# Kernel optimization log

Hardware: AMD Instinct MI355X
Metric: run time of the kernel (lower is better)

The kernel has to match this reference:

```python
import jax, jax.numpy as jnp
import numpy as np

B, N, C_IN, C_OUT, K = 8, 1024, 64, 64, 4


def setup_inputs() -> dict:
    key = jax.random.key(0)
    k1, k2, k3 = jax.random.split(key, 3)
    x = jax.random.normal(k1, (B, N, C_IN), dtype=jnp.float32)
    # scaled-Laplacian-like matrix; 1/sqrt(N) scaling keeps Chebyshev recurrence stable
    L = jax.random.normal(k2, (B, N, N), dtype=jnp.float32) * (1.0 / np.sqrt(N))
    theta = jax.random.normal(k3, (K, C_IN, C_OUT), dtype=jnp.float32) * np.sqrt(2.0 / C_IN)
    return {"x": x, "L": L, "theta": theta}


def reference(x, L, theta):
    # Chebyshev recurrence applied directly to feature vectors:
    #   z0 = x, z1 = L x, z_k = 2 L z_{k-1} - z_{k-2}
    # out = sum_k z_k @ theta[k]  -- same math as materializing T_k(L),
    # since T_k(L) @ x obeys the same 3-term recurrence.
    k_orders = theta.shape[0]
    z_prev = x                      # [B,N,C]
    out = jnp.matmul(z_prev, theta[0])
    if k_orders > 1:
        z_curr = jnp.matmul(L, x)   # [B,N,C]
        out = out + jnp.matmul(z_curr, theta[1])
        for k in range(2, k_orders):
            z_next = 2.0 * jnp.matmul(L, z_curr) - z_prev
            out = out + jnp.matmul(z_next, theta[k])
            z_prev, z_curr = z_curr, z_next
    return out
```

## Files before the change

kernel.cpp:

```cpp
#include <hip/hip_runtime.h>
#include <cstdint>
#include <cstddef>


typedef __bf16 bf16;
typedef bf16 bf16x4 __attribute__((ext_vector_type(4)));
typedef bf16 bf16x8 __attribute__((ext_vector_type(8)));
typedef float f32x4 __attribute__((ext_vector_type(4)));

#define MFMA_BF16(a, b, c) __builtin_amdgcn_mfma_f32_16x16x32_bf16((a), (b), (c), 0, 0, 0)
#define WAITV(n) asm volatile("s_waitcnt vmcnt(" #n ")" ::: "memory")

__device__ __forceinline__ void dma16(const void* g, void* l) {
    __builtin_amdgcn_global_load_lds(
        (const __attribute__((address_space(1))) unsigned int*)g,
        (__attribute__((address_space(3))) unsigned int*)l, 16, 0, 0);
}

__global__ __launch_bounds__(256) void prep_kernel(const float* __restrict__ x,
                                                   const float* __restrict__ theta,
                                                   const float* __restrict__ Lmat,
                                                   bf16* __restrict__ xT,
                                                   bf16* __restrict__ xb,
                                                   bf16* __restrict__ thT,
                                                   bf16* __restrict__ Lb)
{
    const int bid = blockIdx.x;
    const int t = threadIdx.x;

    if (bid >= 132) {
        constexpr int CHUNKS = (8 * 1024 * 1024) / 4;
        const int stride = (1156 - 132) * 256;
        for (int idx = (bid - 132) * 256 + t; idx < CHUNKS; idx += stride) {
            f32x4 v = ((const f32x4*)Lmat)[idx];
            bf16x4 q;
#pragma unroll
            for (int i = 0; i < 4; ++i) q[i] = (bf16)v[i];
            ((bf16x4*)Lb)[idx] = q;
        }
        return;
    }

    __shared__ bf16 tile[64][72];
    const int r = t >> 2;
    const int c0 = (t & 3) << 4;
    const float* src;
    bf16* dstT;
    int dst_ld;
    const bool isx = bid < 128;
    int b = 0, n0 = 0;
    if (isx) {
        b = bid >> 4; n0 = (bid & 15) << 6;
        src = x + (size_t)(b * 1024 + n0) * 64;
        dstT = xT + (size_t)b * 64 * 1024 + n0;
        dst_ld = 1024;
    } else {
        const int k = bid - 128;
        src = theta + (size_t)k * 4096;
        dstT = thT + (size_t)k * 4096;
        dst_ld = 64;
    }

    bf16x8 row0, row1;
#pragma unroll
    for (int j = 0; j < 16; j += 4) {
        f32x4 v = *reinterpret_cast<const f32x4*>(src + r * 64 + c0 + j);
#pragma unroll
        for (int i = 0; i < 4; ++i) {
            bf16 q = (bf16)v[i];
            tile[r][c0 + j + i] = q;
            if (j + i < 8) row0[j + i] = q; else row1[j + i - 8] = q;
        }
    }
    if (isx) {
        bf16* xr = xb + (size_t)(b * 1024 + n0 + r) * 64 + c0;
        *reinterpret_cast<bf16x8*>(xr) = row0;
        *reinterpret_cast<bf16x8*>(xr + 8) = row1;
    }
    __syncthreads();
    bf16x8 o0, o1;
#pragma unroll
    for (int j = 0; j < 8; ++j) { o0[j] = tile[c0 + j][r]; o1[j] = tile[c0 + 8 + j][r]; }
    *reinterpret_cast<bf16x8*>(dstT + (size_t)r * dst_ld + c0) = o0;
    *reinterpret_cast<bf16x8*>(dstT + (size_t)r * dst_ld + c0 + 8) = o1;
}

template <int STAGE>
__global__ __launch_bounds__(256) void stage_kernel(
    const bf16* __restrict__ Lb,
    const bf16* __restrict__ xb,
    const bf16* __restrict__ zinT,
    const bf16* __restrict__ zprevT,
    const bf16* __restrict__ thT,
    bf16* __restrict__ zoutT,
    float* __restrict__ out)
{
    constexpr int D = 5, T = 16, KS = 64, LSTG = 10240;
    __shared__ __align__(16) unsigned char smem[D * LSTG + 16 * 72 * 2];

    const int bid = blockIdx.x;
    const int b  = bid >> 6;
    const int m0 = (bid & 63) << 4;
    const int t  = threadIdx.x;
    const int w  = t >> 6;
    const int l  = t & 63;
    const int l15 = l & 15;
    const int lg  = l >> 4;
    const int c0  = w << 4;

    const bf16* Lrb = Lb + ((size_t)(b * 1024 + m0)) * 1024;
    const bf16* zb  = zinT + (size_t)b * 64 * 1024;

    const int Lg = (w << 5) + (l & 31);
    const int Lrow = Lg >> 3, Lslot = Lg & 7;
    const bf16* Lsrc = Lrb + (size_t)Lrow * 1024 + (Lslot ^ (Lrow & 7)) * 8;
    const int Zg0 = (w << 7) + l, Zg1 = Zg0 + 64;
    const int Zch0 = Zg0 >> 3, Zch1 = Zg1 >> 3;
    const bf16* Zsrc0 = zb + (size_t)Zch0 * 1024 + ((Zg0 & 7) ^ (Zch0 & 7)) * 8;
    const bf16* Zsrc1 = zb + (size_t)Zch1 * 1024 + ((Zg1 & 7) ^ (Zch1 & 7)) * 8;

    auto issue = [&](int k0, unsigned char* bufb) {
        dma16(Zsrc0 + k0, bufb + 2048 + (w << 11));
        dma16(Zsrc1 + k0, bufb + 2048 + (w << 11) + 1024);
        if (l < 32)
            dma16(Lsrc + k0, bufb + (w << 9));
    };

    f32x4 acc = {0.f, 0.f, 0.f, 0.f};

    auto computeStep = [&](const unsigned char* bufb) {
        const bf16* Ll = (const bf16*)bufb;
        const bf16* Zl = (const bf16*)(bufb + 2048);
        const int chan = c0 + l15;
        const int sA = chan & 7;
        bf16x8 a0 = *(const bf16x8*)(Zl + (((chan << 3) + (lg ^ sA)) << 3));
        bf16x8 a1 = *(const bf16x8*)(Zl + (((chan << 3) + ((4 + lg) ^ sA)) << 3));
        const int sB = l15 & 7;
        bf16x8 b0 = *(const bf16x8*)(Ll + (((l15 << 3) + (lg ^ sB)) << 3));
        bf16x8 b1 = *(const bf16x8*)(Ll + (((l15 << 3) + ((4 + lg) ^ sB)) << 3));
        acc = MFMA_BF16(a0, b0, acc);
        acc = MFMA_BF16(a1, b1, acc);
    };

#pragma unroll
    for (int s = 0; s < D - 1; ++s)
        issue(s * KS, smem + s * LSTG);

#pragma unroll
    for (int tt = 0; tt < T; ++tt) {
        const int rem = (T - 1 - tt) < (D - 2) ? (T - 1 - tt) : (D - 2);
        if (rem >= 3)      WAITV(9);
        else if (rem == 2) WAITV(6);
        else if (rem == 1) WAITV(3);
        else               WAITV(0);
        __builtin_amdgcn_sched_barrier(0);
        __builtin_amdgcn_s_barrier();
        __builtin_amdgcn_sched_barrier(0);
        computeStep(smem + (tt % D) * LSTG);
        if (tt + D - 1 < T)
            issue((tt + D - 1) * KS, smem + ((tt + D - 1) % D) * LSTG);
    }

    bf16 (*zbuf)[72] = (bf16(*)[72])(smem + D * LSTG);
    const int cr = c0 + (lg << 2);
    const float alpha = (STAGE == 1) ? 1.0f : 2.0f;
    float zv[4];
#pragma unroll
    for (int r = 0; r < 4; ++r) {
        float zp = 0.f;
        if constexpr (STAGE >= 2)
            zp = (float)zprevT[(size_t)(b * 64 + cr + r) * 1024 + m0 + l15];
        zv[r] = alpha * acc[r] - zp;
    }
    if constexpr (STAGE <= 2) {
#pragma unroll
        for (int r = 0; r < 4; ++r)
            zoutT[(size_t)(b * 64 + cr + r) * 1024 + m0 + l15] = (bf16)zv[r];
    }
#pragma unroll
    for (int r = 0; r < 4; ++r)
        zbuf[l15][cr + r] = (bf16)zv[r];
    __syncthreads();

    const int o = (w << 4) + l15;
    f32x4 oacc;
    if constexpr (STAGE == 1) {
        oacc = (f32x4){0.f, 0.f, 0.f, 0.f};
#pragma unroll
        for (int ck = 0; ck < 2; ++ck) {
            bf16x8 ax = *reinterpret_cast<const bf16x8*>(
                xb + (size_t)(b * 1024 + m0 + l15) * 64 + ck * 32 + lg * 8);
            bf16x8 bt = *reinterpret_cast<const bf16x8*>(
                thT + (size_t)o * 64 + ck * 32 + lg * 8);
            oacc = MFMA_BF16(ax, bt, oacc);
        }
    } else {
#pragma unroll
        for (int r = 0; r < 4; ++r)
            oacc[r] = out[(size_t)(b * 1024 + m0 + lg * 4 + r) * 64 + o];
    }
    constexpr int KTH = (STAGE == 1) ? 1 : STAGE;
#pragma unroll
    for (int ck = 0; ck < 2; ++ck) {
        bf16x8 az = *reinterpret_cast<const bf16x8*>(&zbuf[l15][ck * 32 + lg * 8]);
        bf16x8 bt = *reinterpret_cast<const bf16x8*>(
            thT + (size_t)(KTH * 64 + o) * 64 + ck * 32 + lg * 8);
        oacc = MFMA_BF16(az, bt, oacc);
    }
#pragma unroll
    for (int r = 0; r < 4; ++r)
        out[(size_t)(b * 1024 + m0 + lg * 4 + r) * 64 + o] = oacc[r];
}

extern "C" void kernel_launch(void* const* d_in, const int* in_sizes, int n_in,
                              void* d_out, int out_size, void* d_ws, size_t ws_size,
                              hipStream_t stream)
{
    const float* x  = (const float*)d_in[0];
    const float* L  = (const float*)d_in[1];
    const float* th = (const float*)d_in[2];
    float* out = (float*)d_out;

    bf16* xT  = (bf16*)d_ws;
    bf16* xb  = xT  + (size_t)8 * 64 * 1024;
    bf16* z1T = xb  + (size_t)8 * 64 * 1024;
    bf16* z2T = z1T + (size_t)8 * 64 * 1024;
    bf16* thT = z2T + (size_t)8 * 64 * 1024;
    bf16* Lb  = thT + (size_t)4 * 64 * 64;

    prep_kernel<<<dim3(1156), dim3(256), 0, stream>>>(x, th, L, xT, xb, thT, Lb);
    stage_kernel<1><<<dim3(512), dim3(256), 0, stream>>>(Lb, xb, xT, nullptr, thT, z1T, out);
    stage_kernel<2><<<dim3(512), dim3(256), 0, stream>>>(Lb, xb, z1T, xT, thT, z2T, out);
    stage_kernel<3><<<dim3(512), dim3(256), 0, stream>>>(Lb, xb, z2T, z1T, thT, nullptr, out);
}
```

Baseline: 101.7 us.

## Double row tile per block to reuse Z loads, widen L conversion vectors

Result: no change. 99.73 us (-1.9%).

```diff
diff --git a/kernel.cpp b/kernel.cpp
--- a/kernel.cpp
+++ b/kernel.cpp
@@ -4,7 +4,6 @@
 
 
 typedef __bf16 bf16;
-typedef bf16 bf16x4 __attribute__((ext_vector_type(4)));
 typedef bf16 bf16x8 __attribute__((ext_vector_type(8)));
 typedef float f32x4 __attribute__((ext_vector_type(4)));
 
@@ -29,14 +28,15 @@
     const int t = threadIdx.x;
 
     if (bid >= 132) {
-        constexpr int CHUNKS = (8 * 1024 * 1024) / 4;
+        constexpr int CHUNKS = (8 * 1024 * 1024) / 8;
         const int stride = (1156 - 132) * 256;
         for (int idx = (bid - 132) * 256 + t; idx < CHUNKS; idx += stride) {
-            f32x4 v = ((const f32x4*)Lmat)[idx];
-            bf16x4 q;
-#pragma unroll
-            for (int i = 0; i < 4; ++i) q[i] = (bf16)v[i];
-            ((bf16x4*)Lb)[idx] = q;
+            f32x4 v0 = ((const f32x4*)Lmat)[2 * idx];
+            f32x4 v1 = ((const f32x4*)Lmat)[2 * idx + 1];
+            bf16x8 q;
+#pragma unroll
+            for (int i = 0; i < 4; ++i) { q[i] = (bf16)v0[i]; q[4 + i] = (bf16)v1[i]; }
+            ((bf16x8*)Lb)[idx] = q;
         }
         return;
     }
@@ -86,7 +86,7 @@
 }
 
 template <int STAGE>
-__global__ __launch_bounds__(256) void stage_kernel(
+__global__ __launch_bounds__(512) void stage_kernel(
     const bf16* __restrict__ Lb,
     const bf16* __restrict__ xb,
     const bf16* __restrict__ zinT,
@@ -95,18 +95,19 @@
     bf16* __restrict__ zoutT,
     float* __restrict__ out)
 {
-    constexpr int D = 5, T = 16, KS = 64, LSTG = 10240;
-    __shared__ __align__(16) unsigned char smem[D * LSTG + 16 * 72 * 2];
+    constexpr int D = 5, T = 16, KS = 64, LSTG = 12288;
+    __shared__ __align__(16) unsigned char smem[D * LSTG];
 
     const int bid = blockIdx.x;
-    const int b  = bid >> 6;
-    const int m0 = (bid & 63) << 4;
+    const int b  = bid >> 5;
+    const int m0 = (bid & 31) << 5;
     const int t  = threadIdx.x;
     const int w  = t >> 6;
     const int l  = t & 63;
     const int l15 = l & 15;
     const int lg  = l >> 4;
-    const int c0  = w << 4;
+    const int wq  = w & 3;
+    const int h   = w >> 2;
 
     const bf16* Lrb = Lb + ((size_t)(b * 1024 + m0)) * 1024;
     const bf16* zb  = zinT + (size_t)b * 64 * 1024;
@@ -114,14 +115,12 @@
     const int Lg = (w << 5) + (l & 31);
     const int Lrow = Lg >> 3, Lslot = Lg & 7;
     const bf16* Lsrc = Lrb + (size_t)Lrow * 1024 + (Lslot ^ (Lrow & 7)) * 8;
-    const int Zg0 = (w << 7) + l, Zg1 = Zg0 + 64;
-    const int Zch0 = Zg0 >> 3, Zch1 = Zg1 >> 3;
-    const bf16* Zsrc0 = zb + (size_t)Zch0 * 1024 + ((Zg0 & 7) ^ (Zch0 & 7)) * 8;
-    const bf16* Zsrc1 = zb + (size_t)Zch1 * 1024 + ((Zg1 & 7) ^ (Zch1 & 7)) * 8;
+    const int Zg = (w << 6) + l;
+    const int Zch = Zg >> 3;
+    const bf16* Zsrc = zb + (size_t)Zch * 1024 + ((Zg & 7) ^ (Zch & 7)) * 8;
 
     auto issue = [&](int k0, unsigned char* bufb) {
-        dma16(Zsrc0 + k0, bufb + 2048 + (w << 11));
-        dma16(Zsrc1 + k0, bufb + 2048 + (w << 11) + 1024);
+        dma16(Zsrc + k0, bufb + 4096 + (w << 10));
         if (l < 32)
             dma16(Lsrc + k0, bufb + (w << 9));
     };
@@ -130,14 +129,15 @@
 
     auto computeStep = [&](const unsigned char* bufb) {
         const bf16* Ll = (const bf16*)bufb;
-        const bf16* Zl = (const bf16*)(bufb + 2048);
-        const int chan = c0 + l15;
+        const bf16* Zl = (const bf16*)(bufb + 4096);
+        const int chan = (wq << 4) + l15;
         const int sA = chan & 7;
         bf16x8 a0 = *(const bf16x8*)(Zl + (((chan << 3) + (lg ^ sA)) << 3));
         bf16x8 a1 = *(const bf16x8*)(Zl + (((chan << 3) + ((4 + lg) ^ sA)) << 3));
-        const int sB = l15 & 7;
-        bf16x8 b0 = *(const bf16x8*)(Ll + (((l15 << 3) + (lg ^ sB)) << 3));
-        bf16x8 b1 = *(const bf16x8*)(Ll + (((l15 << 3) + ((4 + lg) ^ sB)) << 3));
+        const int mrow = (h << 4) + l15;
+        const int sB = mrow & 7;
+        bf16x8 b0 = *(const bf16x8*)(Ll + (((mrow << 3) + (lg ^ sB)) << 3));
+        bf16x8 b1 = *(const bf16x8*)(Ll + (((mrow << 3) + ((4 + lg) ^ sB)) << 3));
         acc = MFMA_BF16(a0, b0, acc);
         acc = MFMA_BF16(a1, b1, acc);
     };
@@ -148,10 +148,10 @@
 
 #pragma unroll
     for (int tt = 0; tt < T; ++tt) {
-        const int rem = (T - 1 - tt) < (D - 2) ? (T - 1 - tt) : (D - 2);
-        if (rem >= 3)      WAITV(9);
-        else if (rem == 2) WAITV(6);
-        else if (rem == 1) WAITV(3);
+        const int rem = ((T - tt) < (D - 1) ? (T - tt) : (D - 1)) - 1;
+        if (rem >= 3)      WAITV(6);
+        else if (rem == 2) WAITV(4);
+        else if (rem == 1) WAITV(2);
         else               WAITV(0);
         __builtin_amdgcn_sched_barrier(0);
         __builtin_amdgcn_s_barrier();
@@ -161,35 +161,37 @@
             issue((tt + D - 1) * KS, smem + ((tt + D - 1) % D) * LSTG);
     }
 
-    bf16 (*zbuf)[72] = (bf16(*)[72])(smem + D * LSTG);
-    const int cr = c0 + (lg << 2);
+    bf16 (*zbuf)[72] = (bf16(*)[72])(smem + LSTG);
+    const int cr   = (wq << 4) + (lg << 2);
+    const int mcol = m0 + (h << 4) + l15;
     const float alpha = (STAGE == 1) ? 1.0f : 2.0f;
     float zv[4];
 #pragma unroll
     for (int r = 0; r < 4; ++r) {
         float zp = 0.f;
         if constexpr (STAGE >= 2)
-            zp = (float)zprevT[(size_t)(b * 64 + cr + r) * 1024 + m0 + l15];
+            zp = (float)zprevT[(size_t)(b * 64 + cr + r) * 1024 + mcol];
         zv[r] = alpha * acc[r] - zp;
     }
     if constexpr (STAGE <= 2) {
 #pragma unroll
         for (int r = 0; r < 4; ++r)
-            zoutT[(size_t)(b * 64 + cr + r) * 1024 + m0 + l15] = (bf16)zv[r];
+            zoutT[(size_t)(b * 64 + cr + r) * 1024 + mcol] = (bf16)zv[r];
     }
 #pragma unroll
     for (int r = 0; r < 4; ++r)
-        zbuf[l15][cr + r] = (bf16)zv[r];
+        zbuf[(h << 4) + l15][cr + r] = (bf16)zv[r];
     __syncthreads();
 
-    const int o = (w << 4) + l15;
+    const int o = (wq << 4) + l15;
+    const int mrowA = m0 + (h << 4) + l15;
     f32x4 oacc;
     if constexpr (STAGE == 1) {
         oacc = (f32x4){0.f, 0.f, 0.f, 0.f};
 #pragma unroll
         for (int ck = 0; ck < 2; ++ck) {
             bf16x8 ax = *reinterpret_cast<const bf16x8*>(
-                xb + (size_t)(b * 1024 + m0 + l15) * 64 + ck * 32 + lg * 8);
+                xb + (size_t)(b * 1024 + mrowA) * 64 + ck * 32 + lg * 8);
             bf16x8 bt = *reinterpret_cast<const bf16x8*>(
                 thT + (size_t)o * 64 + ck * 32 + lg * 8);
             oacc = MFMA_BF16(ax, bt, oacc);
@@ -197,19 +199,20 @@
     } else {
 #pragma unroll
         for (int r = 0; r < 4; ++r)
-            oacc[r] = out[(size_t)(b * 1024 + m0 + lg * 4 + r) * 64 + o];
+            oacc[r] = out[(size_t)(b * 1024 + m0 + (h << 4) + lg * 4 + r) * 64 + o];
     }
     constexpr int KTH = (STAGE == 1) ? 1 : STAGE;
 #pragma unroll
     for (int ck = 0; ck < 2; ++ck) {
-        bf16x8 az = *reinterpret_cast<const bf16x8*>(&zbuf[l15][ck * 32 + lg * 8]);
+        bf16x8 az = *reinterpret_cast<const bf16x8*>(
+            &zbuf[(h << 4) + l15][ck * 32 + lg * 8]);
         bf16x8 bt = *reinterpret_cast<const bf16x8*>(
             thT + (size_t)(KTH * 64 + o) * 64 + ck * 32 + lg * 8);
         oacc = MFMA_BF16(az, bt, oacc);
     }
 #pragma unroll
     for (int r = 0; r < 4; ++r)
-        out[(size_t)(b * 1024 + m0 + lg * 4 + r) * 64 + o] = oacc[r];
+        out[(size_t)(b * 1024 + m0 + (h << 4) + lg * 4 + r) * 64 + o] = oacc[r];
 }
 
 extern "C" void kernel_launch(void* const* d_in, const int* in_sizes, int n_in,
@@ -229,7 +232,7 @@
     bf16* Lb  = thT + (size_t)4 * 64 * 64;
 
     prep_kernel<<<dim3(1156), dim3(256), 0, stream>>>(x, th, L, xT, xb, thT, Lb);
-    stage_kernel<1><<<dim3(512), dim3(256), 0, stream>>>(Lb, xb, xT, nullptr, thT, z1T, out);
-    stage_kernel<2><<<dim3(512), dim3(256), 0, stream>>>(Lb, xb, z1T, xT, thT, z2T, out);
-    stage_kernel<3><<<dim3(512), dim3(256), 0, stream>>>(Lb, xb, z2T, z1T, thT, nullptr, out);
-}
+    stage_kernel<1><<<dim3(256), dim3(512), 0, stream>>>(Lb, xb, xT, nullptr, thT, z1T, out);
+    stage_kernel<2><<<dim3(256), dim3(512), 0, stream>>>(Lb, xb, z1T, xT, thT, z2T, out);
+    stage_kernel<3><<<dim3(256), dim3(512), 0, stream>>>(Lb, xb, z2T, z1T, thT, nullptr, out);
+}
```
